# Kernel optimization log

Measured on AMD Instinct MI355X. Metric: run time of the kernel, lower is better.

## Reference

```python
import jax, jax.numpy as jnp
import numpy as np

BIGINT = 1e10

def sinusoidal_embed(pos, dim):
    # SinusoidalPositionEmbedding: interleaved sin/cos, matches torch reshape order
    idx = jnp.arange(dim // 2, dtype=jnp.float32)
    freq = jnp.power(10000.0, -2.0 * idx / dim)
    ang = pos.astype(jnp.float32)[:, None] * freq[None, :]          # [N, d/2]
    emb = jnp.stack([jnp.sin(ang), jnp.cos(ang)], axis=-1)          # [N, d/2, 2]
    return emb.reshape(pos.shape[0], dim)

def dihedral(a, b, c, d):
    # standard signed dihedral angle of four points, [...,3] -> [...]
    u1, u2, u3 = b - a, c - b, d - c
    n1 = jnp.cross(u1, u2)
    n2 = jnp.cross(u2, u3)
    u2n = u2 / (jnp.linalg.norm(u2, axis=-1, keepdims=True) + 1e-12)
    m = jnp.cross(n1, u2n)
    x = jnp.sum(n1 * n2, axis=-1)
    y = jnp.sum(m * n2, axis=-1)
    return jnp.arctan2(y, x)

def knn_edges(X, Seg, bid, k):
    # faithful dense formulation of _construct_knn: pairwise min-over-channel-pair
    # distance, masked by (same bid) & (same Seg), then smallest-k per row.
    N = X.shape[0]
    rule = (bid[:, None] == bid[None, :]) & (Seg[:, None] == Seg[None, :])  # [N,N]
    sq = jnp.sum(X * X, axis=-1)                                   # [N,C]
    dot = jnp.einsum('icd,jed->icje', X, X)                        # [N,C,N,C]
    d2 = sq[:, :, None, None] + sq[None, None, :, :] - 2.0 * dot   # [N,C,N,C]
    dmin = jnp.sqrt(jnp.maximum(jnp.min(d2, axis=(1, 3)), 0.0))    # [N,N]
    dist = jnp.where(rule, dmin, BIGINT)
    neg_vals, dst = jax.lax.top_k(-dist, k)                        # smallest-k
    dnb = -neg_vals                                                # [N,k]
    src = jnp.broadcast_to(jnp.arange(N)[:, None], (N, k))
    valid = (dnb < BIGINT).reshape(-1)                             # [N*k]
    dst = dst.reshape(-1)
    src = src.reshape(-1)
    # torch compacts invalid edges (dynamic shape); we pad them with -1 + mask
    edges = jnp.stack([jnp.where(valid, dst, -1), jnp.where(valid, src, -1)])
    return edges, valid

def pairwise_dihedrals(X, dst, src):
    # inter-residue dihedrals on backbone atoms, channels = [N, CA, C, O]
    ir_phi = dihedral(X[dst, 2], X[src, 0], X[src, 1], X[src, 2])  # C_i, N_j, CA_j, C_j
    ir_psi = dihedral(X[dst, 0], X[dst, 1], X[dst, 2], X[src, 0])  # N_i, CA_i, C_i, N_j
    return jnp.stack([ir_phi, ir_psi], axis=-1)                    # [E, 2]

def setup_inputs() -> dict:
    key = jax.random.key(0)
    ks = jax.random.split(key, 8)
    N, C, E, NUM_AA, NUM_ID = 3000, 4, 64, 21, 2
    X = jax.random.normal(ks[0], (N, C, 3), dtype=jnp.float32) * 10.0
    S = jax.random.randint(ks[1], (N,), 0, NUM_AA)
    RP = jax.random.randint(ks[2], (N,), 0, 1000)
    ID = jax.random.randint(ks[3], (N,), 0, NUM_ID)
    Seg = jax.random.randint(ks[4], (N,), 0, 2)
    bid = jnp.sort(jax.random.randint(ks[5], (N,), 0, 8))
    res_embed = jax.random.normal(ks[6], (NUM_AA, E), dtype=jnp.float32)
    id_embed = jax.random.normal(ks[7], (NUM_ID, E), dtype=jnp.float32)
    return {"X": X, "S": S, "RP": RP, "ID": ID, "Seg": Seg, "bid": bid,
            "res_embed": res_embed, "id_embed": id_embed, "k_neighbors": 10}

def reference(X, S, RP, ID, Seg, bid, res_embed, id_embed, k_neighbors):
    # node features: [residue embedding, positional + chain-id embedding]
    res_h = res_embed[S]                                           # [N,E]
    rp_h = sinusoidal_embed(RP, res_embed.shape[1]) + id_embed[ID] # [N,E]
    H = jnp.concatenate([res_h, rp_h], axis=-1)                    # [N,2E]
    edges, valid = knn_edges(X, Seg, bid, k_neighbors)             # [2,N*k], [N*k]
    dst = jnp.maximum(edges[0], 0)
    src = jnp.maximum(edges[1], 0)
    edge_attr = pairwise_dihedrals(X, dst, src)                    # [N*k,2]
    edge_attr = jnp.where(valid[:, None], edge_attr, 0.0)
    return H, edges, edge_attr, valid
```

## Files before the change

### kernel.cpp

```cpp
#include <hip/hip_runtime.h>
#include <math.h>

#define TOPK 10
#define WAVE 64
#define MAXC 256
#define MAXM 4

__device__ __forceinline__ void cross3(const float* a, const float* b, float* o) {
    o[0] = a[1] * b[2] - a[2] * b[1];
    o[1] = a[2] * b[0] - a[0] * b[2];
    o[2] = a[0] * b[1] - a[1] * b[0];
}
__device__ __forceinline__ float dot3(const float* a, const float* b) {
    return a[0] * b[0] + a[1] * b[1] + a[2] * b[2];
}

__device__ float dihedral4(const float* a, const float* b, const float* c, const float* d) {
    float u1[3], u2[3], u3[3];
    #pragma unroll
    for (int t = 0; t < 3; t++) {
        u1[t] = b[t] - a[t];
        u2[t] = c[t] - b[t];
        u3[t] = d[t] - c[t];
    }
    float n1[3], n2[3];
    cross3(u1, u2, n1);
    cross3(u2, u3, n2);
    float nrm = sqrtf(dot3(u2, u2)) + 1e-12f;
    float u2n[3] = {u2[0] / nrm, u2[1] / nrm, u2[2] / nrm};
    float m[3];
    cross3(n1, u2n, m);
    float x = dot3(n1, n2);
    float y = dot3(m, n2);
    return atan2f(y, x);
}

__device__ __forceinline__ void load_xrow(const float4* __restrict__ X4, int j,
                                          float xj[4][3]) {
    float4 a = X4[j * 3 + 0];
    float4 b = X4[j * 3 + 1];
    float4 c = X4[j * 3 + 2];
    xj[0][0] = a.x; xj[0][1] = a.y; xj[0][2] = a.z;
    xj[1][0] = a.w; xj[1][1] = b.x; xj[1][2] = b.y;
    xj[2][0] = b.z; xj[2][1] = b.w; xj[2][2] = c.x;
    xj[3][0] = c.y; xj[3][1] = c.z; xj[3][2] = c.w;
}

template <int M>
__device__ __forceinline__ void rank_all(const unsigned long long* __restrict__ keys,
                                         int cnt, const unsigned long long own[MAXM],
                                         int rank[MAXM]) {
    const ulonglong2* k2 = (const ulonglong2*)keys;
    const int quads = cnt >> 2;
    for (int q = 0; q < quads; q++) {
        ulonglong2 ka = k2[2 * q + 0];
        ulonglong2 kb = k2[2 * q + 1];
        #pragma unroll
        for (int m = 0; m < M; m++) {
            rank[m] += (ka.x < own[m]) ? 1 : 0;
            rank[m] += (ka.y < own[m]) ? 1 : 0;
            rank[m] += (kb.x < own[m]) ? 1 : 0;
            rank[m] += (kb.y < own[m]) ? 1 : 0;
        }
    }
    for (int r = quads << 2; r < cnt; r++) {
        unsigned long long kr = keys[r];
        #pragma unroll
        for (int m = 0; m < M; m++) rank[m] += (kr < own[m]) ? 1 : 0;
    }
}

__device__ __forceinline__ int find_first(const int* __restrict__ bid, int s, int e,
                                          int b, bool strict, int dflt, int lane) {
    int q = s + lane;
    bool in = (q <= e);
    int v = in ? bid[q] : 0;
    bool pred = in && (strict ? (v > b) : (v >= b));
    unsigned long long m = __ballot(pred);
    if (m == 0ull) return dflt;
    return s + (int)(__ffsll((long long)m) - 1);
}

__global__ __launch_bounds__(WAVE) void fused_graph_kernel(
    const float* __restrict__ X,
    const int* __restrict__ S,
    const int* __restrict__ RP,
    const int* __restrict__ ID,
    const int* __restrict__ Seg,
    const int* __restrict__ bid,
    const float* __restrict__ res_embed,
    const float* __restrict__ id_embed,
    float* __restrict__ H,
    float* __restrict__ out_e0,
    float* __restrict__ out_e1,
    float* __restrict__ out_attr,
    float* __restrict__ out_valid,
    int N, int E) {
    __shared__ __align__(16) unsigned long long keys[MAXC];

    const int i = blockIdx.x;
    const int lane = threadIdx.x;
    const float4* X4 = (const float4*)X;

    {
        float* Hrow = H + (size_t)i * 2 * E;
        Hrow[lane] = res_embed[S[i] * E + lane];
        if (lane < E / 2) {
            int half = lane;
            float freq = exp2f((float)half * (-2.0f * 13.287712379549449f / 64.0f));
            float ang = (float)RP[i] * freq;
            float s, c;
            __sincosf(ang, &s, &c);
            const float2 idv = *(const float2*)(id_embed + ID[i] * E + 2 * half);
            float2 o;
            o.x = s + idv.x;
            o.y = c + idv.y;
            *(float2*)(Hrow + E + 2 * half) = o;
        }
    }

    float xi[4][3], sqi[4];
    load_xrow(X4, i, xi);
    #pragma unroll
    for (int c = 0; c < 4; c++)
        sqi[c] = xi[c][0] * xi[c][0] + xi[c][1] * xi[c][1] + xi[c][2] * xi[c][2];

    const int b = bid[i];
    const int segI = Seg[i];

    int p = (lane * N) >> 6;
    int vb = bid[p];
    unsigned long long mge = __ballot(vb >= b);
    unsigned long long mgt = __ballot(vb > b);
    int lo, hi;
    if (mge == 0ull) {
        lo = find_first(bid, ((63 * N) >> 6) + 1, N - 1, b, false, N, lane);
    } else {
        int f = (int)(__ffsll((long long)mge) - 1);
        lo = (f == 0) ? 0
                      : find_first(bid, (((f - 1) * N) >> 6) + 1, (f * N) >> 6, b,
                                   false, N, lane);
    }
    if (mgt == 0ull) {
        hi = find_first(bid, ((63 * N) >> 6) + 1, N - 1, b, true, N, lane);
    } else {
        int f = (int)(__ffsll((long long)mgt) - 1);
        hi = find_first(bid, (((f - 1) * N) >> 6) + 1, (f * N) >> 6, b, true, N, lane);
    }

    const unsigned long long EMPTY = ~0ull;
    int cbase = 0;
    for (int base = lo; base < hi; base += WAVE) {
        int t = base + lane;
        bool act = false;
        unsigned long long key = EMPTY;
        if (t < hi && Seg[t] == segI) {
            act = true;
            float xj[4][3], sqj[4];
            load_xrow(X4, t, xj);
            #pragma unroll
            for (int c = 0; c < 4; c++)
                sqj[c] = xj[c][0] * xj[c][0] + xj[c][1] * xj[c][1] + xj[c][2] * xj[c][2];

            float bestd2 = 3.4e38f;
            #pragma unroll
            for (int c = 0; c < 4; c++) {
                #pragma unroll
                for (int e = 0; e < 4; e++) {
                    float dp = xi[c][0] * xj[e][0] + xi[c][1] * xj[e][1] +
                               xi[c][2] * xj[e][2];
                    float d2 = (sqi[c] + sqj[e]) - 2.0f * dp;
                    bestd2 = fminf(bestd2, d2);
                }
            }
            float dist = sqrtf(fmaxf(bestd2, 0.0f));
            key = ((unsigned long long)__float_as_uint(dist) << 32) | (unsigned)t;
        }
        unsigned long long mask = __ballot(act);
        int pos = cbase + (int)__popcll(mask & ((1ull << lane) - 1ull));
        if (act && pos < MAXC) keys[pos] = key;
        cbase += (int)__popcll(mask);
    }
    int cnt = (cbase < MAXC) ? cbase : MAXC;

    __syncthreads();

    unsigned long long own[MAXM];
    int rank[MAXM];
    #pragma unroll
    for (int m = 0; m < MAXM; m++) {
        own[m] = EMPTY;
        rank[m] = 0;
    }
    const int m2max = (cnt + WAVE - 1) >> 6;
    #pragma unroll
    for (int m = 0; m < MAXM; m++) {
        int t = m * WAVE + lane;
        if (m < m2max && t < cnt) own[m] = keys[t];
    }

    if (m2max <= 2)
        rank_all<2>(keys, cnt, own, rank);
    else if (m2max == 3)
        rank_all<3>(keys, cnt, own, rank);
    else
        rank_all<4>(keys, cnt, own, rank);

    if (cnt < TOPK && lane >= cnt && lane < TOPK) {
        int e = i * TOPK + lane;
        out_e0[e] = -1.0f;
        out_e1[e] = -1.0f;
        out_valid[e] = 0.0f;
        out_attr[e * 2 + 0] = 0.0f;
        out_attr[e * 2 + 1] = 0.0f;
    }
    #pragma unroll
    for (int m = 0; m < MAXM; m++) {
        if (own[m] != EMPTY && rank[m] < TOPK) {
            int j = (int)(own[m] & 0xffffffffu);
            int e = i * TOPK + rank[m];
            out_e0[e] = (float)j;
            out_e1[e] = (float)i;
            out_valid[e] = 1.0f;
            float xj[4][3];
            load_xrow(X4, j, xj);
            float phi = dihedral4(xj[2], xi[0], xi[1], xi[2]);
            float psi = dihedral4(xj[0], xj[1], xj[2], xi[0]);
            out_attr[e * 2 + 0] = phi;
            out_attr[e * 2 + 1] = psi;
        }
    }
}

extern "C" void kernel_launch(void* const* d_in, const int* in_sizes, int n_in,
                              void* d_out, int out_size, void* d_ws, size_t ws_size,
                              hipStream_t stream) {
    const float* X = (const float*)d_in[0];
    const int* S = (const int*)d_in[1];
    const int* RP = (const int*)d_in[2];
    const int* ID = (const int*)d_in[3];
    const int* Seg = (const int*)d_in[4];
    const int* bid = (const int*)d_in[5];
    const float* res_embed = (const float*)d_in[6];
    const float* id_embed = (const float*)d_in[7];

    const int N = in_sizes[1];
    const int E = 64;

    float* out = (float*)d_out;
    float* H = out;
    float* e0 = H + (size_t)N * 2 * E;
    float* e1 = e0 + (size_t)N * TOPK;
    float* attr = e1 + (size_t)N * TOPK;
    float* validp = attr + (size_t)N * TOPK * 2;

    (void)d_ws;
    (void)ws_size;
    hipLaunchKernelGGL(fused_graph_kernel, dim3(N), dim3(WAVE), 0, stream,
                       X, S, RP, ID, Seg, bid, res_embed, id_embed,
                       H, e0, e1, attr, validp, N, E);
}
```

Baseline: 92.18 us.

## Replace rank-counting top-k with register sort and wave-min selection

The candidate pass now only compacts matching neighbour indices into shared memory. Distances are computed afterwards into per-lane registers, up to four per lane, which are sorted with a small compare-swap network. The top-10 are then extracted with ten 64-bit wave-min shuffle reductions, removing the O(cnt^2) rank-counting loop over shared keys. The trade is serial shuffle reductions and more register-resident state. The output order still follows ascending key.

```diff
diff --git a/kernel.cpp b/kernel.cpp
--- a/kernel.cpp
+++ b/kernel.cpp
@@ -46,28 +46,18 @@
     xj[3][0] = c.y; xj[3][1] = c.z; xj[3][2] = c.w;
 }
 
-template <int M>
-__device__ __forceinline__ void rank_all(const unsigned long long* __restrict__ keys,
-                                         int cnt, const unsigned long long own[MAXM],
-                                         int rank[MAXM]) {
-    const ulonglong2* k2 = (const ulonglong2*)keys;
-    const int quads = cnt >> 2;
-    for (int q = 0; q < quads; q++) {
-        ulonglong2 ka = k2[2 * q + 0];
-        ulonglong2 kb = k2[2 * q + 1];
-        #pragma unroll
-        for (int m = 0; m < M; m++) {
-            rank[m] += (ka.x < own[m]) ? 1 : 0;
-            rank[m] += (ka.y < own[m]) ? 1 : 0;
-            rank[m] += (kb.x < own[m]) ? 1 : 0;
-            rank[m] += (kb.y < own[m]) ? 1 : 0;
-        }
-    }
-    for (int r = quads << 2; r < cnt; r++) {
-        unsigned long long kr = keys[r];
-        #pragma unroll
-        for (int m = 0; m < M; m++) rank[m] += (kr < own[m]) ? 1 : 0;
-    }
+__device__ __forceinline__ unsigned long long u64min(unsigned long long a,
+                                                     unsigned long long b) {
+    return (a < b) ? a : b;
+}
+
+__device__ __forceinline__ unsigned long long wave_min64(unsigned long long v) {
+    #pragma unroll
+    for (int s = 32; s >= 1; s >>= 1) {
+        unsigned long long o = (unsigned long long)__shfl_xor((long long)v, s, WAVE);
+        v = u64min(v, o);
+    }
+    return v;
 }
 
 __device__ __forceinline__ int find_first(const int* __restrict__ bid, int s, int e,
@@ -96,7 +86,8 @@
     float* __restrict__ out_attr,
     float* __restrict__ out_valid,
     int N, int E) {
-    __shared__ __align__(16) unsigned long long keys[MAXC];
+    __shared__ int idxs[MAXC];
+    __shared__ int winj[TOPK];
 
     const int i = blockIdx.x;
     const int lane = threadIdx.x;
@@ -148,16 +139,30 @@
         hi = find_first(bid, (((f - 1) * N) >> 6) + 1, (f * N) >> 6, b, true, N, lane);
     }
 
-    const unsigned long long EMPTY = ~0ull;
     int cbase = 0;
     for (int base = lo; base < hi; base += WAVE) {
         int t = base + lane;
-        bool act = false;
-        unsigned long long key = EMPTY;
-        if (t < hi && Seg[t] == segI) {
-            act = true;
+        bool act = (t < hi) && (Seg[t] == segI);
+        unsigned long long mask = __ballot(act);
+        int pos = cbase + (int)__popcll(mask & ((1ull << lane) - 1ull));
+        if (act && pos < MAXC) idxs[pos] = t;
+        cbase += (int)__popcll(mask);
+    }
+    const int cnt = (cbase < MAXC) ? cbase : MAXC;
+    __syncthreads();
+
+    const unsigned long long EMPTY = ~0ull;
+    unsigned long long own[MAXM];
+    #pragma unroll
+    for (int m = 0; m < MAXM; m++) own[m] = EMPTY;
+
+    const int mmax = (cnt + WAVE - 1) >> 6;
+    for (int m = 0; m < mmax; m++) {
+        int t = m * WAVE + lane;
+        if (t < cnt) {
+            int j = idxs[t];
             float xj[4][3], sqj[4];
-            load_xrow(X4, t, xj);
+            load_xrow(X4, j, xj);
             #pragma unroll
             for (int c = 0; c < 4; c++)
                 sqj[c] = xj[c][0] * xj[c][0] + xj[c][1] * xj[c][1] + xj[c][2] * xj[c][2];
@@ -174,51 +179,39 @@
                 }
             }
             float dist = sqrtf(fmaxf(bestd2, 0.0f));
-            key = ((unsigned long long)__float_as_uint(dist) << 32) | (unsigned)t;
-        }
-        unsigned long long mask = __ballot(act);
-        int pos = cbase + (int)__popcll(mask & ((1ull << lane) - 1ull));
-        if (act && pos < MAXC) keys[pos] = key;
-        cbase += (int)__popcll(mask);
-    }
-    int cnt = (cbase < MAXC) ? cbase : MAXC;
-
+            own[m] = ((unsigned long long)__float_as_uint(dist) << 32) | (unsigned)j;
+        }
+    }
+
+    {
+        unsigned long long t;
+        #define CSWAP(a, bq)                                   \
+            if (own[bq] < own[a]) {                            \
+                t = own[a]; own[a] = own[bq]; own[bq] = t;     \
+            }
+        CSWAP(0, 1) CSWAP(2, 3) CSWAP(0, 2) CSWAP(1, 3) CSWAP(1, 2)
+        #undef CSWAP
+    }
+
+    int nk = 0;
+    for (int k = 0; k < TOPK; k++) {
+        unsigned long long wm = wave_min64(own[0]);
+        if (wm == EMPTY) break;
+        if (own[0] == wm) {
+            winj[k] = (int)(wm & 0xffffffffu);
+            own[0] = own[1];
+            own[1] = own[2];
+            own[2] = own[3];
+            own[3] = EMPTY;
+        }
+        nk = k + 1;
+    }
     __syncthreads();
 
-    unsigned long long own[MAXM];
-    int rank[MAXM];
-    #pragma unroll
-    for (int m = 0; m < MAXM; m++) {
-        own[m] = EMPTY;
-        rank[m] = 0;
-    }
-    const int m2max = (cnt + WAVE - 1) >> 6;
-    #pragma unroll
-    for (int m = 0; m < MAXM; m++) {
-        int t = m * WAVE + lane;
-        if (m < m2max && t < cnt) own[m] = keys[t];
-    }
-
-    if (m2max <= 2)
-        rank_all<2>(keys, cnt, own, rank);
-    else if (m2max == 3)
-        rank_all<3>(keys, cnt, own, rank);
-    else
-        rank_all<4>(keys, cnt, own, rank);
-
-    if (cnt < TOPK && lane >= cnt && lane < TOPK) {
+    if (lane < TOPK) {
         int e = i * TOPK + lane;
-        out_e0[e] = -1.0f;
-        out_e1[e] = -1.0f;
-        out_valid[e] = 0.0f;
-        out_attr[e * 2 + 0] = 0.0f;
-        out_attr[e * 2 + 1] = 0.0f;
-    }
-    #pragma unroll
-    for (int m = 0; m < MAXM; m++) {
-        if (own[m] != EMPTY && rank[m] < TOPK) {
-            int j = (int)(own[m] & 0xffffffffu);
-            int e = i * TOPK + rank[m];
+        if (lane < nk) {
+            int j = winj[lane];
             out_e0[e] = (float)j;
             out_e1[e] = (float)i;
             out_valid[e] = 1.0f;
@@ -228,6 +221,12 @@
             float psi = dihedral4(xj[0], xj[1], xj[2], xi[0]);
             out_attr[e * 2 + 0] = phi;
             out_attr[e * 2 + 1] = psi;
+        } else {
+            out_e0[e] = -1.0f;
+            out_e1[e] = -1.0f;
+            out_valid[e] = 0.0f;
+            out_attr[e * 2 + 0] = 0.0f;
+            out_attr[e * 2 + 1] = 0.0f;
         }
     }
 }
```

Result: faster. 82.94 us (-10.0%).
